# Performance work log

Measured on AMD Instinct MI355X. Metric: run time of the kernel, lower is better.

## Reference

```python
import jax, jax.numpy as jnp
import numpy as np

N_NODES = 100000
N_EDGES = 400000
D = 128

def _mlp_ln(x, W1, b1, W2, b2, W3, b3, gamma, beta):
    h = jax.nn.relu(x @ W1 + b1)
    h = jax.nn.relu(h @ W2 + b2)
    h = h @ W3 + b3
    mu = jnp.mean(h, axis=-1, keepdims=True)
    var = jnp.var(h, axis=-1, keepdims=True)
    return (h - mu) * jax.lax.rsqrt(var + 1e-5) * gamma + beta


def setup_inputs() -> dict:
    key = jax.random.key(0)
    ks = jax.random.split(key, 12)
    s = lambda fan_in: 1.0 / np.sqrt(fan_in)
    inp = {
        'node_features': jax.random.normal(ks[0], (1, N_NODES, D), jnp.float32),
        'edge_features': jax.random.normal(ks[1], (1, N_EDGES, D), jnp.float32),
        'senders': jax.random.randint(ks[2], (1, N_EDGES), 0, N_NODES, jnp.int32),
        'receivers': jax.random.randint(ks[3], (1, N_EDGES), 0, N_NODES, jnp.int32),
        'e_W1': jax.random.normal(ks[4], (3 * D, D), jnp.float32) * s(3 * D),
        'e_b1': jnp.zeros((D,), jnp.float32),
        'e_W2': jax.random.normal(ks[5], (D, D), jnp.float32) * s(D),
        'e_b2': jnp.zeros((D,), jnp.float32),
        'e_W3': jax.random.normal(ks[6], (D, D), jnp.float32) * s(D),
        'e_b3': jnp.zeros((D,), jnp.float32),
        'e_gamma': jnp.ones((D,), jnp.float32),
        'e_beta': jnp.zeros((D,), jnp.float32),
        'n_W1': jax.random.normal(ks[7], (2 * D, D), jnp.float32) * s(2 * D),
        'n_b1': jnp.zeros((D,), jnp.float32),
        'n_W2': jax.random.normal(ks[8], (D, D), jnp.float32) * s(D),
        'n_b2': jnp.zeros((D,), jnp.float32),
        'n_W3': jax.random.normal(ks[9], (D, D), jnp.float32) * s(D),
        'n_b3': jnp.zeros((D,), jnp.float32),
        'n_gamma': jnp.ones((D,), jnp.float32),
        'n_beta': jnp.zeros((D,), jnp.float32),
    }
    return inp


def reference(node_features, edge_features, senders, receivers,
              e_W1, e_b1, e_W2, e_b2, e_W3, e_b3, e_gamma, e_beta,
              n_W1, n_b1, n_W2, n_b2, n_W3, n_b3, n_gamma, n_beta):
    # batch dim is 1; indexing matches torch.index_select(dim=1, senders[0])
    snd = senders[0]
    rcv = receivers[0]
    nodes = node_features[0]          # [N, D]
    edges = edge_features[0]          # [E, D]

    # edge update: gather, concat, edge MLP
    edge_in = jnp.concatenate([nodes[snd], nodes[rcv], edges], axis=-1)  # [E, 3D]
    new_edges = _mlp_ln(edge_in, e_W1, e_b1, e_W2, e_b2, e_W3, e_b3, e_gamma, e_beta)

    # node update: segment-sum aggregate to receivers, concat, node MLP
    agg = jax.ops.segment_sum(new_edges, rcv, num_segments=nodes.shape[0])  # [N, D]
    node_in = jnp.concatenate([nodes, agg], axis=-1)                        # [N, 2D]
    new_nodes = _mlp_ln(node_in, n_W1, n_b1, n_W2, n_b2, n_W3, n_b3, n_gamma, n_beta)

    # residuals
    new_nodes = new_nodes + nodes
    new_edges = new_edges + edges
    return new_nodes[None], new_edges[None]
```

## Files before the change

### kernel.cpp

```cpp
#include <hip/hip_runtime.h>
#include <stdint.h>

#define NN 100000
#define NE 400000
#define SCAN_B 391

typedef __attribute__((ext_vector_type(4))) float f32x4;
typedef __attribute__((ext_vector_type(8))) short bf16x8;

__device__ __forceinline__ short f2b(float x){
  union { float f; uint32_t u; } v; v.f = x;
  uint32_t r = v.u + 0x7FFFu + ((v.u >> 16) & 1u);
  return (short)(r >> 16);
}
__device__ __forceinline__ float b2f(short x){
  union { uint32_t u; float f; } v; v.u = ((uint32_t)(unsigned short)x) << 16; return v.f;
}
__device__ __forceinline__ bf16x8 pack_bf8(f32x4 a, f32x4 b){
  bf16x8 r;
  r[0]=f2b(a[0]); r[1]=f2b(a[1]); r[2]=f2b(a[2]); r[3]=f2b(a[3]);
  r[4]=f2b(b[0]); r[5]=f2b(b[1]); r[6]=f2b(b[2]); r[7]=f2b(b[3]);
  return r;
}

__global__ void pack_all(const float* __restrict__ eW1, const float* __restrict__ eW2,
                         const float* __restrict__ eW3, const float* __restrict__ nW1,
                         const float* __restrict__ nW2, const float* __restrict__ nW3,
                         short* __restrict__ dst){
  int o = blockIdx.x*256 + threadIdx.x;
  int seg = o >> 14, rem = o & 16383;
  int kt = rem >> 12, g = (rem >> 10) & 3, n = (rem >> 3) & 127, j = rem & 7;
  int k = kt*32 + g*8 + j;
  const float* src = eW1; int koff = 0;
  switch(seg){
    case 0: src=eW1; koff=0;   break;
    case 1: src=eW1; koff=128; break;
    case 2: src=eW1; koff=256; break;
    case 3: src=eW2; break;
    case 4: src=eW3; break;
    case 5: src=nW1; koff=0;   break;
    case 6: src=nW1; koff=128; break;
    case 7: src=nW2; break;
    case 8: src=nW3; break;
  }
  dst[o] = f2b(src[(size_t)(koff+k)*128 + n]);
}

__global__ void k_count(const int* __restrict__ rcv, int* __restrict__ counts){
  int e = blockIdx.x*256 + threadIdx.x;
  if (e < NE) atomicAdd(&counts[rcv[e]], 1);
}
__global__ void k_psum(const int* __restrict__ counts, int* __restrict__ psums){
  __shared__ int red[256];
  int t = threadIdx.x, i = blockIdx.x*256 + t;
  red[t] = (i < NN) ? counts[i] : 0;
  __syncthreads();
  for (int d=128; d; d>>=1){ if (t<d) red[t] += red[t+d]; __syncthreads(); }
  if (!t) psums[blockIdx.x] = red[0];
}
__global__ __launch_bounds__(512) void k_scanp(const int* __restrict__ psums, int* __restrict__ bbase){
  __shared__ int ps[512];
  int t = threadIdx.x;
  int v = (t < SCAN_B) ? psums[t] : 0;
  ps[t] = v; __syncthreads();
  for (int d=1; d<512; d<<=1){
    int x = (t>=d) ? ps[t-d] : 0;
    __syncthreads();
    ps[t] += x;
    __syncthreads();
  }
  if (t < SCAN_B) bbase[t] = ps[t] - v;
}
__global__ void k_local(const int* __restrict__ counts, const int* __restrict__ bbase,
                        int* __restrict__ offsets, int* __restrict__ cursor){
  __shared__ int ps[256];
  int t = threadIdx.x, i = blockIdx.x*256 + t;
  int v = (i < NN) ? counts[i] : 0;
  ps[t] = v; __syncthreads();
  for (int d=1; d<256; d<<=1){
    int x = (t>=d) ? ps[t-d] : 0;
    __syncthreads();
    ps[t] += x;
    __syncthreads();
  }
  int excl = bbase[blockIdx.x] + ps[t] - v;
  if (i < NN){ offsets[i] = excl; cursor[i] = excl; }
  if (i == 0) offsets[NN] = NE;
}
__global__ void k_scatter(const int* __restrict__ rcv, int* __restrict__ cursor,
                          int* __restrict__ pos){
  int e = blockIdx.x*256 + threadIdx.x;
  if (e < NE) pos[e] = atomicAdd(&cursor[rcv[e]], 1);
}

__global__ __launch_bounds__(512,4) void compute_T(
    const float* __restrict__ nodef, const short* __restrict__ wp,
    short* __restrict__ Tt, int nrows)
{
  __shared__ __align__(16) short Ws[16384];
  const int tid=threadIdx.x, lane=tid&63, wid=tid>>6, l16=lane&15, hi=lane>>4;
  const int row0 = blockIdx.x*128;
  const int arow_l = wid*16 + l16;
  const int arow_c = min(row0 + arow_l, nrows-1);
  const float* s = nodef + (size_t)arow_c*128;

  bf16x8 af[4];
  #pragma unroll
  for (int kt=0; kt<4; kt++){
    int ko = kt*32 + hi*8;
    af[kt] = pack_bf8(*(const f32x4*)(s+ko), *(const f32x4*)(s+ko+4));
  }
  int4 w[4];
  #pragma unroll
  for (int i=0;i<4;i++) w[i] = ((const int4*)wp)[tid + 512*i];

  for (int o=0; o<2; o++){
    if (o) __syncthreads();
    #pragma unroll
    for (int i=0;i<4;i++) ((int4*)Ws)[tid + 512*i] = w[i];
    if (o < 1){
      #pragma unroll
      for (int i=0;i<4;i++) w[i] = ((const int4*)(wp + 16384))[tid + 512*i];
    }
    __syncthreads();
    f32x4 acc[8];
    #pragma unroll
    for (int t=0;t<8;t++) acc[t] = (f32x4)(0.0f);
    #pragma unroll
    for (int kt=0;kt<4;kt++){
      #pragma unroll
      for (int t=0;t<8;t++){
        bf16x8 bw = *(const bf16x8*)&Ws[kt*4096 + hi*1024 + (t*16+l16)*8];
        acc[t] = __builtin_amdgcn_mfma_f32_16x16x32_bf16(af[kt], bw, acc[t], 0,0,0);
      }
    }
    __syncthreads();
    #pragma unroll
    for (int t=0;t<8;t++){
      int col = t*16 + l16;
      #pragma unroll
      for (int r=0;r<4;r++){
        int row = wid*16 + hi*4 + r;
        *(short*)((char*)Ws + row*256 + ((col*2) ^ ((row&7)<<4))) = f2b(acc[t][r]);
      }
    }
    #pragma unroll
    for (int u=0;u<4;u++){
      int q = lane + u*64;
      int r16 = q >> 4, c = q & 15;
      int rl = wid*16 + r16;
      int grow = row0 + rl;
      if (grow < nrows){
        bf16x8 v = *(const bf16x8*)((char*)Ws + rl*256 + ((c*16) ^ ((rl&7)<<4)));
        *(bf16x8*)(Tt + (size_t)grow*256 + o*128 + c*8) = v;
      }
    }
  }
}

#define WSTAGE(NEXT) do{ __syncthreads(); \
  _Pragma("unroll") for(int i=0;i<4;i++) ((int4*)Ws)[tid + 512*i] = w[i]; \
  if ((NEXT) != nullptr){ _Pragma("unroll") for(int i=0;i<4;i++) w[i] = ((const int4*)(NEXT))[tid + 512*i]; } \
  __syncthreads(); }while(0)

#define MM_G() do{ _Pragma("unroll") for(int kt=0;kt<4;kt++){ \
  _Pragma("unroll") for(int t=0;t<8;t++){ \
    bf16x8 bw = *(const bf16x8*)&Ws[kt*4096 + hi*1024 + (t*16+l16)*8]; \
    acc[t] = __builtin_amdgcn_mfma_f32_16x16x32_bf16(afg[kt], bw, acc[t], 0,0,0);} } }while(0)

#define MM_H() do{ _Pragma("unroll") for(int kt=0;kt<4;kt++){ \
  bf16x8 afv = *(const bf16x8*)((char*)HGs + arow_l*256 + ((kt*64 + hi*16) ^ ((arow_l&7)<<4))); \
  _Pragma("unroll") for(int t=0;t<8;t++){ \
    bf16x8 bw = *(const bf16x8*)&Ws[kt*4096 + hi*1024 + (t*16+l16)*8]; \
    acc[t] = __builtin_amdgcn_mfma_f32_16x16x32_bf16(afv, bw, acc[t], 0,0,0);} } }while(0)

#define EPI_RELU(BP) do{ \
  _Pragma("unroll") for (int t=0;t<8;t++){ \
    int col=t*16+l16; float bb=(BP)[col]; \
    _Pragma("unroll") for (int r=0;r<4;r++){ \
      int row=wid*16+hi*4+r; \
      float v=fmaxf(acc[t][r]+bb,0.0f); \
      *(short*)((char*)HGs+row*256+((col*2)^((row&7)<<4)))=f2b(v); \
      acc[t][r]=0.0f; \
    } } }while(0)

template<int MODE>
__global__ __launch_bounds__(512,4) void gnb_mlp(
    const float* __restrict__ nodef, const float* __restrict__ edgef,
    const int* __restrict__ snd, const int* __restrict__ rcv,
    const int* __restrict__ off, const int* __restrict__ pos,
    const short* __restrict__ Tt, short* __restrict__ Ey,
    const short* __restrict__ W1a, const short* __restrict__ W1b,
    const short* __restrict__ W2, const short* __restrict__ W3,
    const float* __restrict__ b1p, const float* __restrict__ b2p, const float* __restrict__ b3p,
    const float* __restrict__ gmp, const float* __restrict__ btp,
    float* __restrict__ outp, int nrows)
{
  __shared__ __align__(16) short Ws[16384];
  __shared__ __align__(16) short HGs[16384];

  const int tid=threadIdx.x, lane=tid&63, wid=tid>>6, l16=lane&15, hi=lane>>4;
  const int row0 = blockIdx.x*128;
  const int arow_l = wid*16 + l16;
  const int arow_c = min(row0 + arow_l, nrows-1);

  int4 w[4];
  #pragma unroll
  for (int i=0;i<4;i++) w[i] = ((const int4*)W1a)[tid + 512*i];

  bf16x8 ga[4], gb[4];
  if (MODE==0){
    int si = snd[row0 + arow_l];
    int ri = rcv[row0 + arow_l];
    const short* ts = Tt + (size_t)si*256;
    const short* tr = Tt + (size_t)ri*256 + 128;
    #pragma unroll
    for (int kt=0;kt<4;kt++){
      int ko = kt*32 + hi*8;
      ga[kt] = *(const bf16x8*)(ts + ko);
      gb[kt] = *(const bf16x8*)(tr + ko);
    }
  } else {
    #pragma unroll
    for (int u=0;u<4;u++){
      int q = tid + u*512, gr = q >> 4, c = q & 15;
      int grow = row0 + gr;
      float s8[8] = {0,0,0,0,0,0,0,0};
      if (grow < nrows){
        int jb = off[grow], je = off[grow+1];
        for (int j=jb;j<je;j++){
          bf16x8 v = *(const bf16x8*)(Ey + (size_t)j*128 + c*8);
          #pragma unroll
          for (int k=0;k<8;k++) s8[k] += b2f(v[k]);
        }
      }
      bf16x8 o8;
      #pragma unroll
      for (int k=0;k<8;k++) o8[k] = f2b(s8[k]);
      *(bf16x8*)((char*)HGs + gr*256 + ((c*16) ^ ((gr&7)<<4))) = o8;
    }
  }

  WSTAGE((MODE==0) ? W2 : W1b);

  const float* s1 = (MODE==0) ? (edgef + (size_t)arow_c*128) : (nodef + (size_t)arow_c*128);
  bf16x8 afg[4];
  #pragma unroll
  for (int kt=0;kt<4;kt++){
    int ko = kt*32 + hi*8;
    afg[kt] = pack_bf8(*(const f32x4*)(s1+ko), *(const f32x4*)(s1+ko+4));
  }

  f32x4 acc[8];
  #pragma unroll
  for (int t=0;t<8;t++) acc[t] = (f32x4)(0.0f);

  MM_G();

  if (MODE==0){
    bf16x8 bI[2];
    #pragma unroll
    for (int s=0;s<2;s++){
      bf16x8 z;
      #pragma unroll
      for (int j=0;j<8;j++) z[j] = 0;
      if (hi == 2*s + (l16>>3)) z[l16&7] = (short)0x3F80;
      bI[s] = z;
    }
    #pragma unroll
    for (int kt=0;kt<4;kt++){
      bf16x8 gf;
      #pragma unroll
      for (int j=0;j<8;j++) gf[j] = f2b(b2f(ga[kt][j]) + b2f(gb[kt][j]));
      acc[2*kt+0] = __builtin_amdgcn_mfma_f32_16x16x32_bf16(gf, bI[0], acc[2*kt+0], 0,0,0);
      acc[2*kt+1] = __builtin_amdgcn_mfma_f32_16x16x32_bf16(gf, bI[1], acc[2*kt+1], 0,0,0);
    }
  } else {
    WSTAGE(W2);
    MM_H();
  }
  EPI_RELU(b1p);
  WSTAGE(W3);
  MM_H();
  EPI_RELU(b2p);
  WSTAGE((const short*)nullptr);
  MM_H();

  float ps[4] = {0,0,0,0}, pq[4] = {0,0,0,0};
  #pragma unroll
  for (int t=0;t<8;t++){
    float bb = b3p[t*16+l16];
    #pragma unroll
    for (int r=0;r<4;r++){
      float v = acc[t][r] + bb;
      acc[t][r] = v;
      ps[r] += v; pq[r] += v*v;
    }
  }
  #pragma unroll
  for (int m=1;m<16;m<<=1){
    #pragma unroll
    for (int r=0;r<4;r++){
      ps[r] += __shfl_xor(ps[r], m);
      pq[r] += __shfl_xor(pq[r], m);
    }
  }
  float mu[4], rs[4];
  #pragma unroll
  for (int r=0;r<4;r++){
    mu[r] = ps[r] * (1.0f/128.0f);
    float var = pq[r] * (1.0f/128.0f) - mu[r]*mu[r];
    rs[r] = rsqrtf(var + 1e-5f);
  }

  #pragma unroll
  for (int t=0;t<8;t++){
    int col = t*16 + l16;
    float gm = gmp[col], be = btp[col];
    #pragma unroll
    for (int r=0;r<4;r++){
      float y = (acc[t][r]-mu[r])*rs[r]*gm + be;
      int row = wid*16 + hi*4 + r;
      *(short*)((char*)HGs + row*256 + ((col*2) ^ ((row&7)<<4))) = f2b(y);
    }
  }

  #pragma unroll
  for (int u=0;u<4;u++){
    int q = lane + u*64;
    int r16 = q >> 4, c = q & 15;
    int rl = wid*16 + r16;
    int grow = row0 + rl;
    bf16x8 v = *(const bf16x8*)((char*)HGs + rl*256 + ((c*16) ^ ((rl&7)<<4)));
    if (MODE==0){
      const float* ef = edgef + (size_t)grow*128 + c*8;
      f32x4 e0 = *(const f32x4*)ef, e1 = *(const f32x4*)(ef+4);
      f32x4 o0, o1;
      #pragma unroll
      for (int j=0;j<4;j++){ o0[j] = b2f(v[j]) + e0[j]; o1[j] = b2f(v[j+4]) + e1[j]; }
      float* op = outp + (size_t)grow*128 + c*8;
      *(f32x4*)op = o0; *(f32x4*)(op+4) = o1;
      int p = pos[grow];
      *(bf16x8*)(Ey + (size_t)p*128 + c*8) = v;
    } else {
      if (grow < nrows){
        const float* nf = nodef + (size_t)grow*128 + c*8;
        f32x4 e0 = *(const f32x4*)nf, e1 = *(const f32x4*)(nf+4);
        f32x4 o0, o1;
        #pragma unroll
        for (int j=0;j<4;j++){ o0[j] = b2f(v[j]) + e0[j]; o1[j] = b2f(v[j+4]) + e1[j]; }
        float* op = outp + (size_t)grow*128 + c*8;
        *(f32x4*)op = o0; *(f32x4*)(op+4) = o1;
      }
    }
  }
}

extern "C" void kernel_launch(void* const* d_in, const int* in_sizes, int n_in,
                              void* d_out, int out_size, void* d_ws, size_t ws_size,
                              hipStream_t stream)
{
  (void)in_sizes; (void)n_in; (void)out_size; (void)ws_size;
  const float* nodef = (const float*)d_in[0];
  const float* edgef = (const float*)d_in[1];
  const int*   snd   = (const int*)d_in[2];
  const int*   rcv   = (const int*)d_in[3];
  const float* eW1 = (const float*)d_in[4];
  const float* eb1 = (const float*)d_in[5];
  const float* eW2 = (const float*)d_in[6];
  const float* eb2 = (const float*)d_in[7];
  const float* eW3 = (const float*)d_in[8];
  const float* eb3 = (const float*)d_in[9];
  const float* egm = (const float*)d_in[10];
  const float* ebt = (const float*)d_in[11];
  const float* nW1 = (const float*)d_in[12];
  const float* nb1 = (const float*)d_in[13];
  const float* nW2 = (const float*)d_in[14];
  const float* nb2 = (const float*)d_in[15];
  const float* nW3 = (const float*)d_in[16];
  const float* nb3 = (const float*)d_in[17];
  const float* ngm = (const float*)d_in[18];
  const float* nbt = (const float*)d_in[19];

  char* wsb = (char*)d_ws;
  short* Tt = (short*)wsb;
  short* Ey = (short*)(wsb + (size_t)NN*256*2);
  int* counts  = (int*)(wsb + (size_t)NN*256*2 + (size_t)NE*128*2);
  int* offsets = counts + NN;
  int* cursor  = offsets + NN + 8;
  int* psums   = cursor + NN;
  int* bbase   = psums + 512;
  int* pos     = bbase + 512;
  short* wp    = (short*)(pos + NE);

  hipMemsetAsync(counts, 0, (size_t)NN*4, stream);
  k_count<<<(NE+255)/256,256,0,stream>>>(rcv, counts);
  k_psum<<<SCAN_B,256,0,stream>>>(counts, psums);
  k_scanp<<<1,512,0,stream>>>(psums, bbase);
  k_local<<<SCAN_B,256,0,stream>>>(counts, bbase, offsets, cursor);
  k_scatter<<<(NE+255)/256,256,0,stream>>>(rcv, cursor, pos);

  pack_all<<<576,256,0,stream>>>(eW1,eW2,eW3,nW1,nW2,nW3,wp);
  compute_T<<<(NN+127)/128,512,0,stream>>>(nodef, wp, Tt, NN);

  float* out_nodes = (float*)d_out;
  float* out_edges = out_nodes + (size_t)NN*128;

  gnb_mlp<0><<<NE/128,512,0,stream>>>(nodef, edgef, snd, rcv, offsets, pos, Tt, Ey,
      wp+2*16384, (const short*)nullptr, wp+3*16384, wp+4*16384,
      eb1,eb2,eb3, egm,ebt, out_edges, NE);
  gnb_mlp<1><<<(NN+127)/128,512,0,stream>>>(nodef, edgef, snd, rcv, offsets, pos, Tt, Ey,
      wp+5*16384, wp+6*16384, wp+7*16384, wp+8*16384,
      nb1,nb2,nb3, ngm,nbt, out_nodes, NN);
}
```

Before: 446.3 us.

## Halve MLP block to 64 rows and stage weights in half-K chunks

The fused edge/node MLP kernel now runs 256-thread blocks covering 64 rows, with half-size shared buffers for weights and activations. Each 128x128 weight matrix is staged in two 64-row K halves, with a sync and half-matmul per stage. This cuts shared memory per block so more blocks can be resident, at the cost of twice as many __syncthreads and weight stagings per layer, and each weight byte is reloaded by twice as many blocks.

```diff
diff --git a/kernel.cpp b/kernel.cpp
--- a/kernel.cpp
+++ b/kernel.cpp
@@ -159,19 +159,19 @@
 }
 
 #define WSTAGE(NEXT) do{ __syncthreads(); \
-  _Pragma("unroll") for(int i=0;i<4;i++) ((int4*)Ws)[tid + 512*i] = w[i]; \
-  if ((NEXT) != nullptr){ _Pragma("unroll") for(int i=0;i<4;i++) w[i] = ((const int4*)(NEXT))[tid + 512*i]; } \
+  _Pragma("unroll") for(int i=0;i<4;i++) ((int4*)Ws)[tid + 256*i] = w[i]; \
+  if ((NEXT) != nullptr){ _Pragma("unroll") for(int i=0;i<4;i++) w[i] = ((const int4*)(NEXT))[tid + 256*i]; } \
   __syncthreads(); }while(0)
 
-#define MM_G() do{ _Pragma("unroll") for(int kt=0;kt<4;kt++){ \
+#define MM_G(KT0) do{ _Pragma("unroll") for(int kk=0;kk<2;kk++){ \
   _Pragma("unroll") for(int t=0;t<8;t++){ \
-    bf16x8 bw = *(const bf16x8*)&Ws[kt*4096 + hi*1024 + (t*16+l16)*8]; \
-    acc[t] = __builtin_amdgcn_mfma_f32_16x16x32_bf16(afg[kt], bw, acc[t], 0,0,0);} } }while(0)
-
-#define MM_H() do{ _Pragma("unroll") for(int kt=0;kt<4;kt++){ \
+    bf16x8 bw = *(const bf16x8*)&Ws[kk*4096 + hi*1024 + (t*16+l16)*8]; \
+    acc[t] = __builtin_amdgcn_mfma_f32_16x16x32_bf16(afg[(KT0)+kk], bw, acc[t], 0,0,0);} } }while(0)
+
+#define MM_H(KT0) do{ _Pragma("unroll") for(int kk=0;kk<2;kk++){ int kt=(KT0)+kk; \
   bf16x8 afv = *(const bf16x8*)((char*)HGs + arow_l*256 + ((kt*64 + hi*16) ^ ((arow_l&7)<<4))); \
   _Pragma("unroll") for(int t=0;t<8;t++){ \
-    bf16x8 bw = *(const bf16x8*)&Ws[kt*4096 + hi*1024 + (t*16+l16)*8]; \
+    bf16x8 bw = *(const bf16x8*)&Ws[kk*4096 + hi*1024 + (t*16+l16)*8]; \
     acc[t] = __builtin_amdgcn_mfma_f32_16x16x32_bf16(afv, bw, acc[t], 0,0,0);} } }while(0)
 
 #define EPI_RELU(BP) do{ \
@@ -185,7 +185,7 @@
     } } }while(0)
 
 template<int MODE>
-__global__ __launch_bounds__(512,4) void gnb_mlp(
+__global__ __launch_bounds__(256,4) void gnb_mlp(
     const float* __restrict__ nodef, const float* __restrict__ edgef,
     const int* __restrict__ snd, const int* __restrict__ rcv,
     const int* __restrict__ off, const int* __restrict__ pos,
@@ -196,17 +196,17 @@
     const float* __restrict__ gmp, const float* __restrict__ btp,
     float* __restrict__ outp, int nrows)
 {
-  __shared__ __align__(16) short Ws[16384];
-  __shared__ __align__(16) short HGs[16384];
+  __shared__ __align__(16) short Ws[8192];
+  __shared__ __align__(16) short HGs[8192];
 
   const int tid=threadIdx.x, lane=tid&63, wid=tid>>6, l16=lane&15, hi=lane>>4;
-  const int row0 = blockIdx.x*128;
+  const int row0 = blockIdx.x*64;
   const int arow_l = wid*16 + l16;
   const int arow_c = min(row0 + arow_l, nrows-1);
 
   int4 w[4];
   #pragma unroll
-  for (int i=0;i<4;i++) w[i] = ((const int4*)W1a)[tid + 512*i];
+  for (int i=0;i<4;i++) w[i] = ((const int4*)W1a)[tid + 256*i];
 
   bf16x8 ga[4], gb[4];
   if (MODE==0){
@@ -223,8 +223,10 @@
   } else {
     #pragma unroll
     for (int u=0;u<4;u++){
-      int q = tid + u*512, gr = q >> 4, c = q & 15;
-      int grow = row0 + gr;
+      int q = lane + u*64;
+      int r16 = q >> 4, c = q & 15;
+      int rl = wid*16 + r16;
+      int grow = row0 + rl;
       float s8[8] = {0,0,0,0,0,0,0,0};
       if (grow < nrows){
         int jb = off[grow], je = off[grow+1];
@@ -237,11 +239,9 @@
       bf16x8 o8;
       #pragma unroll
       for (int k=0;k<8;k++) o8[k] = f2b(s8[k]);
-      *(bf16x8*)((char*)HGs + gr*256 + ((c*16) ^ ((gr&7)<<4))) = o8;
-    }
-  }
-
-  WSTAGE((MODE==0) ? W2 : W1b);
+      *(bf16x8*)((char*)HGs + rl*256 + ((c*16) ^ ((rl&7)<<4))) = o8;
+    }
+  }
 
   const float* s1 = (MODE==0) ? (edgef + (size_t)arow_c*128) : (nodef + (size_t)arow_c*128);
   bf16x8 afg[4];
@@ -255,36 +255,46 @@
   #pragma unroll
   for (int t=0;t<8;t++) acc[t] = (f32x4)(0.0f);
 
-  MM_G();
-
   if (MODE==0){
-    bf16x8 bI[2];
-    #pragma unroll
-    for (int s=0;s<2;s++){
-      bf16x8 z;
-      #pragma unroll
-      for (int j=0;j<8;j++) z[j] = 0;
-      if (hi == 2*s + (l16>>3)) z[l16&7] = (short)0x3F80;
-      bI[s] = z;
-    }
-    #pragma unroll
-    for (int kt=0;kt<4;kt++){
-      bf16x8 gf;
-      #pragma unroll
-      for (int j=0;j<8;j++) gf[j] = f2b(b2f(ga[kt][j]) + b2f(gb[kt][j]));
-      acc[2*kt+0] = __builtin_amdgcn_mfma_f32_16x16x32_bf16(gf, bI[0], acc[2*kt+0], 0,0,0);
-      acc[2*kt+1] = __builtin_amdgcn_mfma_f32_16x16x32_bf16(gf, bI[1], acc[2*kt+1], 0,0,0);
-    }
+    WSTAGE(W1a+8192); MM_G(0);
+    WSTAGE(W2);       MM_G(2);
+    {
+      bf16x8 bI[2];
+      #pragma unroll
+      for (int s=0;s<2;s++){
+        bf16x8 z;
+        #pragma unroll
+        for (int j=0;j<8;j++) z[j] = 0;
+        if (hi == 2*s + (l16>>3)) z[l16&7] = (short)0x3F80;
+        bI[s] = z;
+      }
+      #pragma unroll
+      for (int kt=0;kt<4;kt++){
+        bf16x8 gf;
+        #pragma unroll
+        for (int j=0;j<8;j++) gf[j] = f2b(b2f(ga[kt][j]) + b2f(gb[kt][j]));
+        acc[2*kt+0] = __builtin_amdgcn_mfma_f32_16x16x32_bf16(gf, bI[0], acc[2*kt+0], 0,0,0);
+        acc[2*kt+1] = __builtin_amdgcn_mfma_f32_16x16x32_bf16(gf, bI[1], acc[2*kt+1], 0,0,0);
+      }
+    }
+    EPI_RELU(b1p);
+    WSTAGE(W2+8192);  MM_H(0);
+    WSTAGE(W3);       MM_H(2);
+    EPI_RELU(b2p);
+    WSTAGE(W3+8192);  MM_H(0);
+    WSTAGE((const short*)nullptr); MM_H(2);
   } else {
-    WSTAGE(W2);
-    MM_H();
-  }
-  EPI_RELU(b1p);
-  WSTAGE(W3);
-  MM_H();
-  EPI_RELU(b2p);
-  WSTAGE((const short*)nullptr);
-  MM_H();
+    WSTAGE(W1a+8192); MM_G(0);
+    WSTAGE(W1b);      MM_G(2);
+    WSTAGE(W1b+8192); MM_H(0);
+    WSTAGE(W2);       MM_H(2);
+    EPI_RELU(b1p);
+    WSTAGE(W2+8192);  MM_H(0);
+    WSTAGE(W3);       MM_H(2);
+    EPI_RELU(b2p);
+    WSTAGE(W3+8192);  MM_H(0);
+    WSTAGE((const short*)nullptr); MM_H(2);
+  }
 
   float ps[4] = {0,0,0,0}, pq[4] = {0,0,0,0};
   #pragma unroll
@@ -406,10 +416,10 @@
   float* out_nodes = (float*)d_out;
   float* out_edges = out_nodes + (size_t)NN*128;
 
-  gnb_mlp<0><<<NE/128,512,0,stream>>>(nodef, edgef, snd, rcv, offsets, pos, Tt, Ey,
+  gnb_mlp<0><<<NE/64,256,0,stream>>>(nodef, edgef, snd, rcv, offsets, pos, Tt, Ey,
       wp+2*16384, (const short*)nullptr, wp+3*16384, wp+4*16384,
       eb1,eb2,eb3, egm,ebt, out_edges, NE);
-  gnb_mlp<1><<<(NN+127)/128,512,0,stream>>>(nodef, edgef, snd, rcv, offsets, pos, Tt, Ey,
+  gnb_mlp<1><<<(NN+63)/64,256,0,stream>>>(nodef, edgef, snd, rcv, offsets, pos, Tt, Ey,
       wp+5*16384, wp+6*16384, wp+7*16384, wp+8*16384,
       nb1,nb2,nb3, ngm,nbt, out_nodes, NN);
 }
```

Result: slower. 594.9 us (+33.3%).
